# Kernel tuning notes

Hardware: AMD Instinct MI355X
Metric: run time of the kernel (lower is better)

## Reference

```python
import jax, jax.numpy as jnp
import numpy as np

G, NPG = 8192, 8            # graphs, nodes per graph (8 sensors, recon head = 8*9)
N = G * NPG                 # 65536 total nodes
IN, HID, HEADS = 9, 64, 4
NEG_SLOPE = 0.2


def _fc_edges():
    # directed fully-connected edges (no self loops) within each 8-node graph
    i, j = np.meshgrid(np.arange(NPG), np.arange(NPG), indexing='ij')
    m = i != j
    src_l, dst_l = i[m], j[m]                       # 56 edges per graph
    off = (np.arange(G) * NPG)[:, None]
    src = (off + src_l[None, :]).ravel()
    dst = (off + dst_l[None, :]).ravel()
    return np.stack([src, dst]).astype(np.int32)    # [2, 458752]


def setup_inputs() -> dict:
    key = jax.random.key(0)
    ks = jax.random.split(key, 30)
    ei = jnp.asarray(_fc_edges())
    E = ei.shape[1]
    p = lambda k, shape, s=0.1: jax.random.normal(ks[k], shape, jnp.float32) * s
    return {
        'x': jax.random.normal(ks[0], (N, IN), jnp.float32),
        'edge_index': ei,
        'edge_weight': jax.random.uniform(ks[1], (E,), jnp.float32),
        'batch': jnp.repeat(jnp.arange(G, dtype=jnp.int32), NPG),
        'W1': p(2, (IN, HEADS * HID)), 'a_src1': p(3, (HEADS, HID)),
        'a_dst1': p(4, (HEADS, HID)), 'We1': p(5, (1, HEADS * HID)),
        'a_e1': p(6, (HEADS, HID)), 'b1': jnp.zeros((HEADS * HID,), jnp.float32),
        'W2': p(7, (HEADS * HID, HID)), 'a_src2': p(8, (1, HID)),
        'a_dst2': p(9, (1, HID)), 'We2': p(10, (1, HID)),
        'a_e2': p(11, (1, HID)), 'b2': jnp.zeros((HID,), jnp.float32),
        # recon head: 64 -> 128 -> 72
        'Wr1': p(12, (HID, 2 * HID)), 'br1': jnp.zeros((2 * HID,), jnp.float32),
        'Wr2': p(13, (2 * HID, 8 * IN)), 'br2': jnp.zeros((8 * IN,), jnp.float32),
        # classify head: 64 -> 32 -> 1
        'Wc1': p(14, (HID, 32)), 'bc1': jnp.zeros((32,), jnp.float32),
        'Wc2': p(15, (32, 1)), 'bc2': jnp.zeros((1,), jnp.float32),
    }


def _gat_conv(x, edge_index, edge_attr, W, a_src, a_dst, We, a_e, bias):
    """PyG GATConv (eval mode): add_self_loops(fill='mean'), edge_dim features."""
    n = x.shape[0]
    heads, ch = a_src.shape
    src, dst = edge_index[0], edge_index[1]
    # self loops with edge_attr = mean of incoming edge_attr per node
    deg = jax.ops.segment_sum(jnp.ones_like(edge_attr[:, :1]), dst, num_segments=n)
    loop_attr = jax.ops.segment_sum(edge_attr, dst, num_segments=n) / jnp.maximum(deg, 1.0)
    src = jnp.concatenate([src, jnp.arange(n, dtype=src.dtype)])
    dst = jnp.concatenate([dst, jnp.arange(n, dtype=dst.dtype)])
    ea = jnp.concatenate([edge_attr, loop_attr], axis=0)          # [E+N, 1]
    xp = (x @ W).reshape(n, heads, ch)                            # [N, H, C]
    al_s = jnp.einsum('nhc,hc->nh', xp, a_src)
    al_d = jnp.einsum('nhc,hc->nh', xp, a_dst)
    ep = (ea @ We).reshape(-1, heads, ch)                         # [E+N, H, C]
    al_e = jnp.einsum('ehc,hc->eh', ep, a_e)
    alpha = al_s[src] + al_d[dst] + al_e                          # [E+N, H]
    alpha = jax.nn.leaky_relu(alpha, NEG_SLOPE)
    # segment softmax over destination nodes
    m = jax.ops.segment_max(alpha, dst, num_segments=n)
    alpha = jnp.exp(alpha - m[dst])
    s = jax.ops.segment_sum(alpha, dst, num_segments=n)
    alpha = alpha / (s[dst] + 1e-16)
    # scatter-aggregate weighted messages
    out = jax.ops.segment_sum(xp[src] * alpha[..., None], dst, num_segments=n)
    return out.reshape(n, heads * ch) + bias


def reference(x, edge_index, edge_weight, batch,
              W1, a_src1, a_dst1, We1, a_e1, b1,
              W2, a_src2, a_dst2, We2, a_e2, b2,
              Wr1, br1, Wr2, br2, Wc1, bc1, Wc2, bc2):
    ew = edge_weight[:, None]
    h = _gat_conv(x, edge_index, ew, W1, a_src1, a_dst1, We1, a_e1, b1)
    h = jax.nn.elu(h)
    h = _gat_conv(h, edge_index, ew, W2, a_src2, a_dst2, We2, a_e2, b2)
    h = jax.nn.elu(h)
    # global mean pool over graphs
    g = G
    cnt = jax.ops.segment_sum(jnp.ones((h.shape[0], 1), h.dtype), batch, num_segments=g)
    emb = jax.ops.segment_sum(h, batch, num_segments=g) / jnp.maximum(cnt, 1.0)
    recon = jax.nn.relu(emb @ Wr1 + br1) @ Wr2 + br2
    cls = jax.nn.relu(emb @ Wc1 + bc1) @ Wc2 + bc2
    return recon, cls
```

## Files before the change

kernel.cpp:

```cpp
#include <hip/hip_runtime.h>
#include <math.h>

#define NEG 0.2f
#define GROUPS 8192

typedef unsigned short u16;
typedef u16 ushort8 __attribute__((ext_vector_type(8)));
typedef short s16x8 __attribute__((ext_vector_type(8)));
typedef float f32x4 __attribute__((ext_vector_type(4)));

__device__ __forceinline__ float lrelu(float x){ return x >= 0.f ? x : NEG*x; }
__device__ __forceinline__ float eluf(float x){ return x > 0.f ? x : __expf(x) - 1.f; }
__device__ __forceinline__ int eidx(int s,int d){ return s*7 + (d<s ? d : d-1); }
__device__ __forceinline__ float bf2f(u16 u){
    union { unsigned i; float f; } v; v.i = ((unsigned)u)<<16; return v.f;
}
__device__ __forceinline__ u16 f2bf(float f){
    union { float f; unsigned i; } v; v.f = f;
    unsigned r = v.i + 0x7fffu + ((v.i>>16)&1u);
    return (u16)(r>>16);
}

__global__ __launch_bounds__(64)
void prep(const float* __restrict__ W1, const float* __restrict__ a_src1,
          const float* __restrict__ a_dst1, const float* __restrict__ W2,
          const float* __restrict__ Wr1, const float* __restrict__ Wr2,
          const float* __restrict__ Wc1,
          const float* __restrict__ We1, const float* __restrict__ a_e1,
          const float* __restrict__ We2, const float* __restrict__ a_e2,
          u16* __restrict__ wfrag, u16* __restrict__ wr1f,
          u16* __restrict__ wr2f, u16* __restrict__ wc1f,
          float* __restrict__ w1s, float* __restrict__ ces)
{
    const int b = blockIdx.x, l = threadIdx.x;
    const int c0 = l & 15, o = l >> 4;
    if (b < 32) {
        const int t = b >> 3, s = b & 7;
        ushort8 p;
#pragma unroll
        for (int j = 0; j < 8; ++j) p[j] = f2bf(W2[(o*64 + s*8 + j)*64 + t*16 + c0]);
        *(ushort8*)(wfrag + (size_t)(b*64 + l)*8) = p;
    } else if (b < 48) {
        const int f = b - 32, ks = f >> 3, t = f & 7;
        ushort8 p;
#pragma unroll
        for (int j = 0; j < 8; ++j) p[j] = f2bf(Wr1[(ks*32 + o*8 + j)*128 + t*16 + c0]);
        *(ushort8*)(wr1f + (size_t)(f*64 + l)*8) = p;
    } else if (b < 68) {
        const int f = b - 48, ks = f / 5, t = f % 5;
        const int c = t*16 + c0;
        ushort8 p;
#pragma unroll
        for (int j = 0; j < 8; ++j)
            p[j] = (c < 72) ? f2bf(Wr2[(ks*32 + o*8 + j)*72 + c]) : (u16)0;
        *(ushort8*)(wr2f + (size_t)(f*64 + l)*8) = p;
    } else if (b < 72) {
        const int f = b - 68, ks = f >> 1, t = f & 1;
        ushort8 p;
#pragma unroll
        for (int j = 0; j < 8; ++j) p[j] = f2bf(Wc1[(ks*32 + o*8 + j)*32 + t*16 + c0]);
        *(ushort8*)(wc1f + (size_t)(f*64 + l)*8) = p;
    } else if (b == 72) {
        for (int idx = l; idx < 72; idx += 64) {
            const int k = idx >> 3, cc = idx & 7, h = cc & 3;
            const float* av = (cc < 4) ? a_src1 : a_dst1;
            float acc = 0.f;
#pragma unroll 8
            for (int i = 0; i < 64; ++i) acc = fmaf(W1[k*256 + h*64 + i], av[h*64 + i], acc);
            w1s[idx] = acc;
        }
    } else {
        if (l < 4) {
            float c = 0.f;
#pragma unroll 8
            for (int i = 0; i < 64; ++i) c = fmaf(We1[l*64+i], a_e1[l*64+i], c);
            ces[l] = c;
        } else if (l == 4) {
            float c = 0.f;
#pragma unroll 8
            for (int i = 0; i < 64; ++i) c = fmaf(We2[i], a_e2[i], c);
            ces[4] = c;
        }
    }
}

__global__ __launch_bounds__(64, 4)
void gat_fused11(const float* __restrict__ x, const float* __restrict__ ew_g,
    const float* __restrict__ W1, const float* __restrict__ b1,
    const float* __restrict__ a_src2, const float* __restrict__ a_dst2,
    const float* __restrict__ b2,
    const float* __restrict__ br1, const float* __restrict__ br2,
    const float* __restrict__ bc1, const float* __restrict__ Wc2,
    const float* __restrict__ bc2,
    const u16* __restrict__ wfrag, const u16* __restrict__ wr1f,
    const u16* __restrict__ wr2f, const u16* __restrict__ wc1f,
    const float* __restrict__ w1s, const float* __restrict__ cesg,
    float* __restrict__ recon, float* __restrict__ cls)
{
    __shared__ __align__(16) float xw[2][72];
    __shared__ float ews2[2][56];
    __shared__ float w1sL[72];
    __shared__ float cesL[6];
    __shared__ __align__(16) float xp2f[2][8][68];
    __shared__ __align__(16) u16 embs16[2][64];
    __shared__ __align__(16) u16 r1s16[2][128];

    const int lane = threadIdx.x;
    const int n    = lane >> 3;
    const int cg   = lane & 7;
    const int g0   = blockIdx.x * 2;
    const int o    = lane >> 4;
    const int rr   = lane & 15;
    const int gA   = rr >> 3, nA = rr & 7;

    {
        const float* xg = x + (size_t)g0 * 72;
        for (int i = lane; i < 144; i += 64) (&xw[0][0])[i] = xg[i];
        const float* eg = ew_g + (size_t)g0 * 56;
        for (int i = lane; i < 112; i += 64) (&ews2[0][0])[i] = eg[i];
        for (int i = lane; i < 72; i += 64) w1sL[i] = w1s[i];
        if (lane < 6) cesL[lane] = cesg[lane];
    }
    __syncthreads();

    float alsv = 0.f, aldv = 0.f;
    {
        const int gg = lane >> 5, nn = (lane >> 2) & 7, hh = lane & 3;
        float s = 0.f, d = 0.f;
#pragma unroll
        for (int k = 0; k < 9; ++k) {
            const float xv = xw[gg][nn*9 + k];
            s = fmaf(xv, w1sL[k*8 + hh], s);
            d = fmaf(xv, w1sL[k*8 + 4 + hh], d);
        }
        alsv = s; aldv = d;
    }

    float lgn[8];
    {
        const int gg = lane >> 5, dd = (lane >> 2) & 7, hh = lane & 3;
        float lw = 0.f;
#pragma unroll
        for (int ss = 0; ss < 8; ++ss) if (ss != dd) lw += ews2[gg][eidx(ss, dd)];
        lw *= (1.f/7.f);
        const float ce = cesL[hh];
        float mx = -1e30f;
#pragma unroll
        for (int ss = 0; ss < 8; ++ss) {
            const float as_ = __shfl(alsv, (lane & 0x23) | (ss << 2));
            const float w = (ss == dd) ? lw : ews2[gg][eidx(ss, dd)];
            float t = as_ + aldv + ce * w;
            t = lrelu(t);
            lgn[ss] = t; mx = fmaxf(mx, t);
        }
        float sum = 0.f;
#pragma unroll
        for (int ss = 0; ss < 8; ++ss) { lgn[ss] = __expf(lgn[ss] - mx); sum += lgn[ss]; }
        const float inv = 1.f / (sum + 1e-16f);
#pragma unroll
        for (int ss = 0; ss < 8; ++ss) lgn[ss] *= inv;
    }

    float y[9];
    {
        const int src = gA*32 + nA*4 + o;
#pragma unroll
        for (int k = 0; k < 9; ++k) y[k] = 0.f;
#pragma unroll
        for (int ss = 0; ss < 8; ++ss) {
            const float av = __shfl(lgn[ss], src);
#pragma unroll
            for (int k = 0; k < 9; ++k) y[k] = fmaf(av, xw[gA][ss*9 + k], y[k]);
        }
    }

    f32x4 acc[4] = {{0,0,0,0},{0,0,0,0},{0,0,0,0},{0,0,0,0}};
#pragma unroll
    for (int s = 0; s < 8; ++s) {
        const int cb = o*64 + s*8;
        float v[8];
        {
            const float4 bb0 = *(const float4*)(b1 + cb);
            const float4 bb1 = *(const float4*)(b1 + cb + 4);
            v[0]=bb0.x; v[1]=bb0.y; v[2]=bb0.z; v[3]=bb0.w;
            v[4]=bb1.x; v[5]=bb1.y; v[6]=bb1.z; v[7]=bb1.w;
        }
#pragma unroll
        for (int k = 0; k < 9; ++k) {
            const float yv = y[k];
            const float4 w0 = *(const float4*)(W1 + k*256 + cb);
            const float4 w1 = *(const float4*)(W1 + k*256 + cb + 4);
            v[0]=fmaf(yv,w0.x,v[0]); v[1]=fmaf(yv,w0.y,v[1]);
            v[2]=fmaf(yv,w0.z,v[2]); v[3]=fmaf(yv,w0.w,v[3]);
            v[4]=fmaf(yv,w1.x,v[4]); v[5]=fmaf(yv,w1.y,v[5]);
            v[6]=fmaf(yv,w1.z,v[6]); v[7]=fmaf(yv,w1.w,v[7]);
        }
        s16x8 A;
#pragma unroll
        for (int j = 0; j < 8; ++j) A[j] = (short)f2bf(eluf(v[j]));
#pragma unroll
        for (int t = 0; t < 4; ++t) {
            const s16x8 bf = *(const s16x8*)(wfrag + (size_t)(((t*8 + s)*64 + lane))*8);
            acc[t] = __builtin_amdgcn_mfma_f32_16x16x32_bf16(A, bf, acc[t], 0, 0, 0);
        }
    }

    float sp[4] = {0,0,0,0}, dp[4] = {0,0,0,0};
    {
        const int c0 = lane & 15;
#pragma unroll
        for (int t = 0; t < 4; ++t) {
            const float as_ = a_src2[t*16 + c0];
            const float ad_ = a_dst2[t*16 + c0];
#pragma unroll
            for (int i = 0; i < 4; ++i) {
                sp[i] = fmaf(acc[t][i], as_, sp[i]);
                dp[i] = fmaf(acc[t][i], ad_, dp[i]);
            }
        }
#pragma unroll
        for (int i = 0; i < 4; ++i) {
            sp[i] += __shfl_xor(sp[i],1); sp[i] += __shfl_xor(sp[i],2);
            sp[i] += __shfl_xor(sp[i],4); sp[i] += __shfl_xor(sp[i],8);
            dp[i] += __shfl_xor(dp[i],1); dp[i] += __shfl_xor(dp[i],2);
            dp[i] += __shfl_xor(dp[i],4); dp[i] += __shfl_xor(dp[i],8);
        }
    }

    float lg2n[8];
    {
        const int g = (lane >> 3) & 1, d = lane & 7;
        float al[8];
#pragma unroll
        for (int ss = 0; ss < 8; ++ss)
            al[ss] = __shfl(sp[ss & 3], (g*2 + (ss >> 2)) * 16);
        const int srcd = (g*2 + (d >> 2)) * 16;
        const float q0 = __shfl(dp[0], srcd), q1 = __shfl(dp[1], srcd);
        const float q2 = __shfl(dp[2], srcd), q3 = __shfl(dp[3], srcd);
        const float ad = (d & 2) ? ((d & 1) ? q3 : q2) : ((d & 1) ? q1 : q0);
        float lw = 0.f;
#pragma unroll
        for (int ss = 0; ss < 8; ++ss) if (ss != d) lw += ews2[g][eidx(ss, d)];
        lw *= (1.f/7.f);
        const float ce = cesL[4];
        float mx = -1e30f;
#pragma unroll
        for (int ss = 0; ss < 8; ++ss) {
            const float w = (ss == d) ? lw : ews2[g][eidx(ss, d)];
            float t = al[ss] + ad + ce * w;
            t = lrelu(t);
            lg2n[ss] = t; mx = fmaxf(mx, t);
        }
        float sum = 0.f;
#pragma unroll
        for (int ss = 0; ss < 8; ++ss) { lg2n[ss] = __expf(lg2n[ss] - mx); sum += lg2n[ss]; }
        const float inv = 1.f / (sum + 1e-16f);
#pragma unroll
        for (int ss = 0; ss < 8; ++ss) lg2n[ss] *= inv;
    }

    {
        const int c0 = lane & 15;
#pragma unroll
        for (int t = 0; t < 4; ++t)
#pragma unroll
            for (int i = 0; i < 4; ++i) {
                const int r = o*4 + i;
                xp2f[r >> 3][r & 7][t*16 + c0] = acc[t][i];
            }
    }
    __syncthreads();

    float h2[2][8];
#pragma unroll
    for (int g = 0; g < 2; ++g) {
        const float* xf = &xp2f[g][0][0];
        const int srcg = g*8 + n;
        float a[8] = {0,0,0,0,0,0,0,0};
#pragma unroll
        for (int ss = 0; ss < 8; ++ss) {
            const float av = __shfl(lg2n[ss], srcg);
            const float4 v0 = *(const float4*)(xf + ss*68 + cg*8);
            const float4 v1 = *(const float4*)(xf + ss*68 + cg*8 + 4);
            a[0]=fmaf(av,v0.x,a[0]); a[1]=fmaf(av,v0.y,a[1]);
            a[2]=fmaf(av,v0.z,a[2]); a[3]=fmaf(av,v0.w,a[3]);
            a[4]=fmaf(av,v1.x,a[4]); a[5]=fmaf(av,v1.y,a[5]);
            a[6]=fmaf(av,v1.z,a[6]); a[7]=fmaf(av,v1.w,a[7]);
        }
        const float4 b0 = *(const float4*)(b2 + cg*8);
        const float4 b1v = *(const float4*)(b2 + cg*8 + 4);
        h2[g][0]=eluf(a[0]+b0.x); h2[g][1]=eluf(a[1]+b0.y);
        h2[g][2]=eluf(a[2]+b0.z); h2[g][3]=eluf(a[3]+b0.w);
        h2[g][4]=eluf(a[4]+b1v.x); h2[g][5]=eluf(a[5]+b1v.y);
        h2[g][6]=eluf(a[6]+b1v.z); h2[g][7]=eluf(a[7]+b1v.w);
    }
#pragma unroll
    for (int g = 0; g < 2; ++g)
#pragma unroll
        for (int j = 0; j < 8; ++j) {
            float v = h2[g][j];
            v += __shfl_xor(v, 8); v += __shfl_xor(v, 16); v += __shfl_xor(v, 32);
            h2[g][j] = v * 0.125f;
        }
    if (n == 0) {
#pragma unroll
        for (int g = 0; g < 2; ++g) {
            ushort8 p;
#pragma unroll
            for (int j = 0; j < 8; ++j) p[j] = f2bf(h2[g][j]);
            *(ushort8*)&embs16[g][lane*8] = p;
        }
    }
    __syncthreads();

    s16x8 aemb0 = {0,0,0,0,0,0,0,0}, aemb1 = {0,0,0,0,0,0,0,0};
    {
        const int r = lane & 15;
        if (r < 2) {
            aemb0 = *(const s16x8*)&embs16[r][o*8];
            aemb1 = *(const s16x8*)&embs16[r][32 + o*8];
        }
    }
#pragma unroll
    for (int half = 0; half < 2; ++half) {
        f32x4 ar[4];
        const f32x4 z = {0,0,0,0};
#pragma unroll
        for (int t = 0; t < 4; ++t) ar[t] = z;
#pragma unroll
        for (int t = 0; t < 4; ++t) {
            const int tt = half*4 + t;
            ar[t] = __builtin_amdgcn_mfma_f32_16x16x32_bf16(
                aemb0, *(const s16x8*)(wr1f + (size_t)((0*8 + tt)*64 + lane)*8), ar[t], 0,0,0);
            ar[t] = __builtin_amdgcn_mfma_f32_16x16x32_bf16(
                aemb1, *(const s16x8*)(wr1f + (size_t)((1*8 + tt)*64 + lane)*8), ar[t], 0,0,0);
        }
        const int c0 = lane & 15;
        if (o == 0) {
#pragma unroll
            for (int t = 0; t < 4; ++t) {
                const int tt = half*4 + t;
                const float bb = br1[tt*16 + c0];
                r1s16[0][tt*16 + c0] = f2bf(fmaxf(ar[t][0] + bb, 0.f));
                r1s16[1][tt*16 + c0] = f2bf(fmaxf(ar[t][1] + bb, 0.f));
            }
        }
    }
    __syncthreads();

    {
        f32x4 ac[5];
        const f32x4 z = {0,0,0,0};
#pragma unroll
        for (int t = 0; t < 5; ++t) ac[t] = z;
        const int r = lane & 15;
#pragma unroll
        for (int ks = 0; ks < 4; ++ks) {
            s16x8 a = {0,0,0,0,0,0,0,0};
            if (r < 2) a = *(const s16x8*)&r1s16[r][ks*32 + o*8];
#pragma unroll
            for (int t = 0; t < 5; ++t)
                ac[t] = __builtin_amdgcn_mfma_f32_16x16x32_bf16(
                    a, *(const s16x8*)(wr2f + (size_t)((ks*5 + t)*64 + lane)*8), ac[t], 0,0,0);
        }
        if (o == 0) {
            const int c0 = r;
#pragma unroll
            for (int t = 0; t < 5; ++t) {
                const int c = t*16 + c0;
                if (c < 72) {
                    const float bb = br2[c];
                    recon[(size_t)g0*72 + c]       = ac[t][0] + bb;
                    recon[(size_t)(g0+1)*72 + c]   = ac[t][1] + bb;
                }
            }
        }
    }

    {
        f32x4 ac[2];
        const f32x4 z = {0,0,0,0};
        ac[0] = z; ac[1] = z;
#pragma unroll
        for (int t = 0; t < 2; ++t) {
            ac[t] = __builtin_amdgcn_mfma_f32_16x16x32_bf16(
                aemb0, *(const s16x8*)(wc1f + (size_t)((0*2 + t)*64 + lane)*8), ac[t], 0,0,0);
            ac[t] = __builtin_amdgcn_mfma_f32_16x16x32_bf16(
                aemb1, *(const s16x8*)(wc1f + (size_t)((1*2 + t)*64 + lane)*8), ac[t], 0,0,0);
        }
        const int c0 = lane & 15;
        const float bb0 = bc1[c0], bb1 = bc1[16 + c0];
        const float wc0 = Wc2[c0], wc1v = Wc2[16 + c0];
        float p0 = fmaxf(ac[0][0] + bb0, 0.f)*wc0 + fmaxf(ac[1][0] + bb1, 0.f)*wc1v;
        float p1 = fmaxf(ac[0][1] + bb0, 0.f)*wc0 + fmaxf(ac[1][1] + bb1, 0.f)*wc1v;
        p0 += __shfl_xor(p0,1); p0 += __shfl_xor(p0,2); p0 += __shfl_xor(p0,4); p0 += __shfl_xor(p0,8);
        p1 += __shfl_xor(p1,1); p1 += __shfl_xor(p1,2); p1 += __shfl_xor(p1,4); p1 += __shfl_xor(p1,8);
        if (lane == 0) { cls[g0] = p0 + bc2[0]; cls[g0+1] = p1 + bc2[0]; }
    }
}

extern "C" void kernel_launch(void* const* d_in, const int* in_sizes, int n_in,
                              void* d_out, int out_size, void* d_ws, size_t ws_size,
                              hipStream_t stream) {
    const float* x      = (const float*)d_in[0];
    const float* ew     = (const float*)d_in[2];
    const float* W1     = (const float*)d_in[4];
    const float* a_src1 = (const float*)d_in[5];
    const float* a_dst1 = (const float*)d_in[6];
    const float* We1    = (const float*)d_in[7];
    const float* a_e1   = (const float*)d_in[8];
    const float* b1     = (const float*)d_in[9];
    const float* W2     = (const float*)d_in[10];
    const float* a_src2 = (const float*)d_in[11];
    const float* a_dst2 = (const float*)d_in[12];
    const float* We2    = (const float*)d_in[13];
    const float* a_e2   = (const float*)d_in[14];
    const float* b2     = (const float*)d_in[15];
    const float* Wr1    = (const float*)d_in[16];
    const float* br1    = (const float*)d_in[17];
    const float* Wr2    = (const float*)d_in[18];
    const float* br2    = (const float*)d_in[19];
    const float* Wc1    = (const float*)d_in[20];
    const float* bc1    = (const float*)d_in[21];
    const float* Wc2    = (const float*)d_in[22];
    const float* bc2    = (const float*)d_in[23];

    float* recon = (float*)d_out;
    float* cls   = (float*)d_out + (size_t)GROUPS * 72;

    char* ws = (char*)d_ws;
    u16*   wfrag = (u16*)(ws + 0);
    u16*   wr1f  = (u16*)(ws + 32768);
    u16*   wr2f  = (u16*)(ws + 49152);
    u16*   wc1f  = (u16*)(ws + 69632);
    float* w1s   = (float*)(ws + 73728);
    float* ces   = (float*)(ws + 74016);

    hipLaunchKernelGGL(prep, dim3(74), dim3(64), 0, stream,
                       W1, a_src1, a_dst1, W2, Wr1, Wr2, Wc1,
                       We1, a_e1, We2, a_e2,
                       wfrag, wr1f, wr2f, wc1f, w1s, ces);

    hipLaunchKernelGGL(gat_fused11, dim3(GROUPS/2), dim3(64), 0, stream,
                       x, ew, W1, b1, a_src2, a_dst2, b2,
                       br1, br2, bc1, Wc2, bc2,
                       wfrag, wr1f, wr2f, wc1f, w1s, ces,
                       recon, cls);
}
```

Before: 44.02 us.

## Process one graph per block and share layer-1 fragments via lane shuffles

The fused GAT kernel now gives each 64-thread block one graph instead of two, doubling the grid and raising the occupancy hint in launch bounds. Rows of the MFMA A-operand duplicate across half-wave lanes, so each lane computes only four of the eight layer-1 fragments and gets the other four with an xor-8 shuffle. The aim is to halve the redundant W1 FMA and ELU work and to raise parallelism and occupancy. In exchange, half the MFMA rows go unused and the weight-fragment loads and setup run twice as often in total.

```diff
diff --git a/kernel.cpp b/kernel.cpp
--- a/kernel.cpp
+++ b/kernel.cpp
@@ -19,6 +19,12 @@
     union { float f; unsigned i; } v; v.f = f;
     unsigned r = v.i + 0x7fffu + ((v.i>>16)&1u);
     return (u16)(r>>16);
+}
+__device__ __forceinline__ s16x8 shflx8(s16x8 v){
+    union { s16x8 s; int i[4]; } u; u.s = v;
+#pragma unroll
+    for (int q = 0; q < 4; ++q) u.i[q] = __shfl_xor(u.i[q], 8);
+    return u.s;
 }
 
 __global__ __launch_bounds__(64)
@@ -84,8 +90,8 @@
     }
 }
 
-__global__ __launch_bounds__(64, 4)
-void gat_fused11(const float* __restrict__ x, const float* __restrict__ ew_g,
+__global__ __launch_bounds__(64, 8)
+void gat_fused13(const float* __restrict__ x, const float* __restrict__ ew_g,
     const float* __restrict__ W1, const float* __restrict__ b1,
     const float* __restrict__ a_src2, const float* __restrict__ a_dst2,
     const float* __restrict__ b2,
@@ -97,27 +103,28 @@
     const float* __restrict__ w1s, const float* __restrict__ cesg,
     float* __restrict__ recon, float* __restrict__ cls)
 {
-    __shared__ __align__(16) float xw[2][72];
-    __shared__ float ews2[2][56];
+    __shared__ __align__(16) float xw[72];
+    __shared__ float ews[56];
     __shared__ float w1sL[72];
     __shared__ float cesL[6];
-    __shared__ __align__(16) float xp2f[2][8][68];
-    __shared__ __align__(16) u16 embs16[2][64];
-    __shared__ __align__(16) u16 r1s16[2][128];
+    __shared__ __align__(16) float xp2f[8][68];
+    __shared__ __align__(16) u16 embs16[64];
+    __shared__ __align__(16) u16 r1s16[128];
 
     const int lane = threadIdx.x;
     const int n    = lane >> 3;
     const int cg   = lane & 7;
-    const int g0   = blockIdx.x * 2;
+    const int g    = blockIdx.x;
     const int o    = lane >> 4;
     const int rr   = lane & 15;
-    const int gA   = rr >> 3, nA = rr & 7;
-
-    {
-        const float* xg = x + (size_t)g0 * 72;
-        for (int i = lane; i < 144; i += 64) (&xw[0][0])[i] = xg[i];
-        const float* eg = ew_g + (size_t)g0 * 56;
-        for (int i = lane; i < 112; i += 64) (&ews2[0][0])[i] = eg[i];
+    const int nC   = rr & 7;
+    const int ph   = rr >> 3;
+
+    {
+        const float* xg = x + (size_t)g * 72;
+        for (int i = lane; i < 72; i += 64) xw[i] = xg[i];
+        const float* eg = ew_g + (size_t)g * 56;
+        if (lane < 56) ews[lane] = eg[lane];
         for (int i = lane; i < 72; i += 64) w1sL[i] = w1s[i];
         if (lane < 6) cesL[lane] = cesg[lane];
     }
@@ -125,11 +132,11 @@
 
     float alsv = 0.f, aldv = 0.f;
     {
-        const int gg = lane >> 5, nn = (lane >> 2) & 7, hh = lane & 3;
+        const int p = lane & 31, nn = p >> 2, hh = p & 3;
         float s = 0.f, d = 0.f;
 #pragma unroll
         for (int k = 0; k < 9; ++k) {
-            const float xv = xw[gg][nn*9 + k];
+            const float xv = xw[nn*9 + k];
             s = fmaf(xv, w1sL[k*8 + hh], s);
             d = fmaf(xv, w1sL[k*8 + 4 + hh], d);
         }
@@ -138,17 +145,17 @@
 
     float lgn[8];
     {
-        const int gg = lane >> 5, dd = (lane >> 2) & 7, hh = lane & 3;
+        const int dd = (lane >> 2) & 7, hh = lane & 3;
         float lw = 0.f;
 #pragma unroll
-        for (int ss = 0; ss < 8; ++ss) if (ss != dd) lw += ews2[gg][eidx(ss, dd)];
+        for (int ss = 0; ss < 8; ++ss) if (ss != dd) lw += ews[eidx(ss, dd)];
         lw *= (1.f/7.f);
         const float ce = cesL[hh];
         float mx = -1e30f;
 #pragma unroll
         for (int ss = 0; ss < 8; ++ss) {
             const float as_ = __shfl(alsv, (lane & 0x23) | (ss << 2));
-            const float w = (ss == dd) ? lw : ews2[gg][eidx(ss, dd)];
+            const float w = (ss == dd) ? lw : ews[eidx(ss, dd)];
             float t = as_ + aldv + ce * w;
             t = lrelu(t);
             lgn[ss] = t; mx = fmaxf(mx, t);
@@ -163,20 +170,21 @@
 
     float y[9];
     {
-        const int src = gA*32 + nA*4 + o;
+        const int src = nC*4 + o;
 #pragma unroll
         for (int k = 0; k < 9; ++k) y[k] = 0.f;
 #pragma unroll
         for (int ss = 0; ss < 8; ++ss) {
             const float av = __shfl(lgn[ss], src);
 #pragma unroll
-            for (int k = 0; k < 9; ++k) y[k] = fmaf(av, xw[gA][ss*9 + k], y[k]);
-        }
-    }
-
-    f32x4 acc[4] = {{0,0,0,0},{0,0,0,0},{0,0,0,0},{0,0,0,0}};
-#pragma unroll
-    for (int s = 0; s < 8; ++s) {
+            for (int k = 0; k < 9; ++k) y[k] = fmaf(av, xw[ss*9 + k], y[k]);
+        }
+    }
+
+    s16x8 frag[4];
+#pragma unroll
+    for (int sl = 0; sl < 4; ++sl) {
+        const int s = ph*4 + sl;
         const int cb = o*64 + s*8;
         float v[8];
         {
@@ -195,9 +203,14 @@
             v[4]=fmaf(yv,w1.x,v[4]); v[5]=fmaf(yv,w1.y,v[5]);
             v[6]=fmaf(yv,w1.z,v[6]); v[7]=fmaf(yv,w1.w,v[7]);
         }
-        s16x8 A;
-#pragma unroll
-        for (int j = 0; j < 8; ++j) A[j] = (short)f2bf(eluf(v[j]));
+#pragma unroll
+        for (int j = 0; j < 8; ++j) frag[sl][j] = (short)f2bf(eluf(v[j]));
+    }
+
+    f32x4 acc[4] = {{0,0,0,0},{0,0,0,0},{0,0,0,0},{0,0,0,0}};
+#pragma unroll
+    for (int s = 0; s < 8; ++s) {
+        const s16x8 A = (s < 4) ? frag[s] : shflx8(frag[s-4]);
 #pragma unroll
         for (int t = 0; t < 4; ++t) {
             const s16x8 bf = *(const s16x8*)(wfrag + (size_t)(((t*8 + s)*64 + lane))*8);
@@ -229,24 +242,24 @@
 
     float lg2n[8];
     {
-        const int g = (lane >> 3) & 1, d = lane & 7;
+        const int d = lane & 7;
         float al[8];
 #pragma unroll
         for (int ss = 0; ss < 8; ++ss)
-            al[ss] = __shfl(sp[ss & 3], (g*2 + (ss >> 2)) * 16);
-        const int srcd = (g*2 + (d >> 2)) * 16;
+            al[ss] = __shfl(sp[ss & 3], (ss >> 2) * 16);
+        const int srcd = (d >> 2) * 16;
         const float q0 = __shfl(dp[0], srcd), q1 = __shfl(dp[1], srcd);
         const float q2 = __shfl(dp[2], srcd), q3 = __shfl(dp[3], srcd);
         const float ad = (d & 2) ? ((d & 1) ? q3 : q2) : ((d & 1) ? q1 : q0);
         float lw = 0.f;
 #pragma unroll
-        for (int ss = 0; ss < 8; ++ss) if (ss != d) lw += ews2[g][eidx(ss, d)];
+        for (int ss = 0; ss < 8; ++ss) if (ss != d) lw += ews[eidx(ss, d)];
         lw *= (1.f/7.f);
         const float ce = cesL[4];
         float mx = -1e30f;
 #pragma unroll
         for (int ss = 0; ss < 8; ++ss) {
-            const float w = (ss == d) ? lw : ews2[g][eidx(ss, d)];
+            const float w = (ss == d) ? lw : ews[eidx(ss, d)];
             float t = al[ss] + ad + ce * w;
             t = lrelu(t);
             lg2n[ss] = t; mx = fmaxf(mx, t);
@@ -259,29 +272,24 @@
         for (int ss = 0; ss < 8; ++ss) lg2n[ss] *= inv;
     }
 
-    {
+    if (o < 2) {
         const int c0 = lane & 15;
 #pragma unroll
         for (int t = 0; t < 4; ++t)
 #pragma unroll
-            for (int i = 0; i < 4; ++i) {
-                const int r = o*4 + i;
-                xp2f[r >> 3][r & 7][t*16 + c0] = acc[t][i];
-            }
+            for (int i = 0; i < 4; ++i)
+                xp2f[o*4 + i][t*16 + c0] = acc[t][i];
     }
     __syncthreads();
 
-    float h2[2][8];
-#pragma unroll
-    for (int g = 0; g < 2; ++g) {
-        const float* xf = &xp2f[g][0][0];
-        const int srcg = g*8 + n;
+    float h2[8];
+    {
         float a[8] = {0,0,0,0,0,0,0,0};
 #pragma unroll
         for (int ss = 0; ss < 8; ++ss) {
-            const float av = __shfl(lg2n[ss], srcg);
-            const float4 v0 = *(const float4*)(xf + ss*68 + cg*8);
-            const float4 v1 = *(const float4*)(xf + ss*68 + cg*8 + 4);
+            const float av = __shfl(lg2n[ss], n);
+            const float4 v0 = *(const float4*)(&xp2f[ss][cg*8]);
+            const float4 v1 = *(const float4*)(&xp2f[ss][cg*8 + 4]);
             a[0]=fmaf(av,v0.x,a[0]); a[1]=fmaf(av,v0.y,a[1]);
             a[2]=fmaf(av,v0.z,a[2]); a[3]=fmaf(av,v0.w,a[3]);
             a[4]=fmaf(av,v1.x,a[4]); a[5]=fmaf(av,v1.y,a[5]);
@@ -289,37 +297,29 @@
         }
         const float4 b0 = *(const float4*)(b2 + cg*8);
         const float4 b1v = *(const float4*)(b2 + cg*8 + 4);
-        h2[g][0]=eluf(a[0]+b0.x); h2[g][1]=eluf(a[1]+b0.y);
-        h2[g][2]=eluf(a[2]+b0.z); h2[g][3]=eluf(a[3]+b0.w);
-        h2[g][4]=eluf(a[4]+b1v.x); h2[g][5]=eluf(a[5]+b1v.y);
-        h2[g][6]=eluf(a[6]+b1v.z); h2[g][7]=eluf(a[7]+b1v.w);
-    }
-#pragma unroll
-    for (int g = 0; g < 2; ++g)
-#pragma unroll
-        for (int j = 0; j < 8; ++j) {
-            float v = h2[g][j];
-            v += __shfl_xor(v, 8); v += __shfl_xor(v, 16); v += __shfl_xor(v, 32);
-            h2[g][j] = v * 0.125f;
-        }
+        h2[0]=eluf(a[0]+b0.x); h2[1]=eluf(a[1]+b0.y);
+        h2[2]=eluf(a[2]+b0.z); h2[3]=eluf(a[3]+b0.w);
+        h2[4]=eluf(a[4]+b1v.x); h2[5]=eluf(a[5]+b1v.y);
+        h2[6]=eluf(a[6]+b1v.z); h2[7]=eluf(a[7]+b1v.w);
+    }
+#pragma unroll
+    for (int j = 0; j < 8; ++j) {
+        float v = h2[j];
+        v += __shfl_xor(v, 8); v += __shfl_xor(v, 16); v += __shfl_xor(v, 32);
+        h2[j] = v * 0.125f;
+    }
     if (n == 0) {
-#pragma unroll
-        for (int g = 0; g < 2; ++g) {
-            ushort8 p;
-#pragma unroll
-            for (int j = 0; j < 8; ++j) p[j] = f2bf(h2[g][j]);
-            *(ushort8*)&embs16[g][lane*8] = p;
-        }
+        ushort8 p;
+#pragma unroll
+        for (int j = 0; j < 8; ++j) p[j] = f2bf(h2[j]);
+        *(ushort8*)&embs16[lane*8] = p;
     }
     __syncthreads();
 
     s16x8 aemb0 = {0,0,0,0,0,0,0,0}, aemb1 = {0,0,0,0,0,0,0,0};
-    {
-        const int r = lane & 15;
-        if (r < 2) {
-            aemb0 = *(const s16x8*)&embs16[r][o*8];
-            aemb1 = *(const s16x8*)&embs16[r][32 + o*8];
-        }
+    if (rr == 0) {
+        aemb0 = *(const s16x8*)&embs16[o*8];
+        aemb1 = *(const s16x8*)&embs16[32 + o*8];
     }
 #pragma unroll
     for (int half = 0; half < 2; ++half) {
@@ -341,8 +341,7 @@
             for (int t = 0; t < 4; ++t) {
                 const int tt = half*4 + t;
                 const float bb = br1[tt*16 + c0];
-                r1s16[0][tt*16 + c0] = f2bf(fmaxf(ar[t][0] + bb, 0.f));
-                r1s16[1][tt*16 + c0] = f2bf(fmaxf(ar[t][1] + bb, 0.f));
+                r1s16[tt*16 + c0] = f2bf(fmaxf(ar[t][0] + bb, 0.f));
             }
         }
     }
@@ -353,26 +352,21 @@
         const f32x4 z = {0,0,0,0};
 #pragma unroll
         for (int t = 0; t < 5; ++t) ac[t] = z;
-        const int r = lane & 15;
 #pragma unroll
         for (int ks = 0; ks < 4; ++ks) {
             s16x8 a = {0,0,0,0,0,0,0,0};
-            if (r < 2) a = *(const s16x8*)&r1s16[r][ks*32 + o*8];
+            if (rr == 0) a = *(const s16x8*)&r1s16[ks*32 + o*8];
 #pragma unroll
             for (int t = 0; t < 5; ++t)
                 ac[t] = __builtin_amdgcn_mfma_f32_16x16x32_bf16(
                     a, *(const s16x8*)(wr2f + (size_t)((ks*5 + t)*64 + lane)*8), ac[t], 0,0,0);
         }
         if (o == 0) {
-            const int c0 = r;
+            const int c0 = lane & 15;
 #pragma unroll
             for (int t = 0; t < 5; ++t) {
                 const int c = t*16 + c0;
-                if (c < 72) {
-                    const float bb = br2[c];
-                    recon[(size_t)g0*72 + c]       = ac[t][0] + bb;
-                    recon[(size_t)(g0+1)*72 + c]   = ac[t][1] + bb;
-                }
+                if (c < 72) recon[(size_t)g*72 + c] = ac[t][0] + br2[c];
             }
         }
     }
@@ -392,10 +386,9 @@
         const float bb0 = bc1[c0], bb1 = bc1[16 + c0];
         const float wc0 = Wc2[c0], wc1v = Wc2[16 + c0];
         float p0 = fmaxf(ac[0][0] + bb0, 0.f)*wc0 + fmaxf(ac[1][0] + bb1, 0.f)*wc1v;
-        float p1 = fmaxf(ac[0][1] + bb0, 0.f)*wc0 + fmaxf(ac[1][1] + bb1, 0.f)*wc1v;
-        p0 += __shfl_xor(p0,1); p0 += __shfl_xor(p0,2); p0 += __shfl_xor(p0,4); p0 += __shfl_xor(p0,8);
-        p1 += __shfl_xor(p1,1); p1 += __shfl_xor(p1,2); p1 += __shfl_xor(p1,4); p1 += __shfl_xor(p1,8);
-        if (lane == 0) { cls[g0] = p0 + bc2[0]; cls[g0+1] = p1 + bc2[0]; }
+        p0 += __shfl_xor(p0,1); p0 += __shfl_xor(p0,2);
+        p0 += __shfl_xor(p0,4); p0 += __shfl_xor(p0,8);
+        if (lane == 0) cls[g] = p0 + bc2[0];
     }
 }
 
@@ -441,7 +434,7 @@
                        We1, a_e1, We2, a_e2,
                        wfrag, wr1f, wr2f, wc1f, w1s, ces);
 
-    hipLaunchKernelGGL(gat_fused11, dim3(GROUPS/2), dim3(64), 0, stream,
+    hipLaunchKernelGGL(gat_fused13, dim3(GROUPS), dim3(64), 0, stream,
                        x, ew, W1, b1, a_src2, a_dst2, b2,
                        br1, br2, bc1, Wc2, bc2,
                        wfrag, wr1f, wr2f, wc1f, w1s, ces,
```

New measurement: 111.4 us. +153.0%, slower.
